# Optimization experiments

Hardware: AMD Instinct MI355X
Metric: run time of the kernel (lower is better)

## Reference

```python
import jax, jax.numpy as jnp
import numpy as np

G = 4          # groups
K = 3          # kernel_size
INC = 64       # channels


def conv3x3(x, w):
    # x: (B, Cin, H, W), w: (Cout, Cin, 3, 3), stride 1, pad 1, no bias
    return jax.lax.conv_general_dilated(
        x, w, window_strides=(1, 1), padding=[(1, 1), (1, 1)],
        dimension_numbers=("NCHW", "OIHW", "NCHW"))


def pconv(x, w):
    # partial conv: 3x3 conv on first C//4 channels, rest untouched
    dc = x.shape[1] // 4
    x1 = conv3x3(x[:, :dc], w)
    return jnp.concatenate([x1, x[:, dc:]], axis=1)


def conv1x1(x, w, b):
    # w: (Cout, Cin), b: (Cout,)
    return jnp.einsum("bchw,oc->bohw", x, w) + b[None, :, None, None]


def deform_sample(img, offset, mask_sig, dilation):
    """Modulated deformable sampling (DSMv3): for each output pixel and each of
    the K*K kernel taps, bilinearly sample img at p + dilated_tap + offset and
    modulate by the (sigmoided) mask. Returns (B, Cg, K*K, H, W)."""
    b, cg, H, W = img.shape
    K2 = K * K
    off = offset.reshape(b, K2, 2, H, W)  # (dy, dx) per tap
    ky = jnp.repeat(jnp.arange(K), K).astype(img.dtype)   # (K2,) row of tap
    kx = jnp.tile(jnp.arange(K), K).astype(img.dtype)     # (K2,) col of tap
    # padding = center*dilation so sampling grid is centered: p = i + (k-1)*dil
    base_y = jnp.arange(H, dtype=img.dtype)[None, :, None] + ((ky - 1.0) * dilation)[:, None, None]  # (K2,H,1)
    base_x = jnp.arange(W, dtype=img.dtype)[None, None, :] + ((kx - 1.0) * dilation)[:, None, None]  # (K2,1,W)
    py = base_y[None] + off[:, :, 0]  # (B,K2,H,W)
    px = base_x[None] + off[:, :, 1]  # (B,K2,H,W)

    y0 = jnp.floor(py)
    x0 = jnp.floor(px)
    wy = py - y0
    wx = px - x0
    imgf = img.reshape(b, cg, H * W)

    def corner(yi, xi, wgt):
        valid = ((yi >= 0) & (yi <= H - 1) & (xi >= 0) & (xi <= W - 1)).astype(img.dtype)
        yc = jnp.clip(yi, 0, H - 1).astype(jnp.int32)
        xc = jnp.clip(xi, 0, W - 1).astype(jnp.int32)
        flat = (yc * W + xc).reshape(b, 1, -1)  # (B,1,K2*H*W)
        v = jnp.take_along_axis(imgf, flat, axis=2).reshape(b, cg, K2, H, W)
        return v * (wgt * valid).reshape(b, 1, K2, H, W)

    val = (corner(y0, x0, (1 - wy) * (1 - wx))
           + corner(y0, x0 + 1, (1 - wy) * wx)
           + corner(y0 + 1, x0, wy * (1 - wx))
           + corner(y0 + 1, x0 + 1, wy * wx))
    return val * mask_sig[:, None]  # (B,Cg,K2,H,W)


def setup_inputs() -> dict:
    key = jax.random.key(0)
    ks = jax.random.split(key, 8)
    dc = INC // 4
    x = jax.random.normal(ks[0], (4, INC, 128, 128), dtype=jnp.float32)
    y = jax.random.normal(ks[1], (8, INC, 128, 128), dtype=jnp.float32)
    # learned params (small random so offsets stay near-zero, as after training warmup)
    offset_pconv_w = jax.random.normal(ks[2], (G, dc, dc, 3, 3), dtype=jnp.float32) * 0.1
    offset_w = jax.random.normal(ks[3], (G, 2 * K * K, INC), dtype=jnp.float32) * 0.1
    offset_b = jax.random.normal(ks[4], (G, 2 * K * K), dtype=jnp.float32) * 0.1
    mask_pconv_w = jax.random.normal(ks[5], (dc, dc, 3, 3), dtype=jnp.float32) * 0.1
    mask_w = jax.random.normal(ks[6], (K * K, INC), dtype=jnp.float32) * 0.1
    mask_b = jax.random.normal(ks[7], (K * K,), dtype=jnp.float32) * 0.1
    return {"x": x, "y": y,
            "offset_pconv_w": offset_pconv_w, "offset_w": offset_w, "offset_b": offset_b,
            "mask_pconv_w": mask_pconv_w, "mask_w": mask_w, "mask_b": mask_b}


def reference(x, y, offset_pconv_w, offset_w, offset_b, mask_pconv_w, mask_w, mask_b):
    b, c, h, w = x.shape
    cg = c // G
    mask = jax.nn.sigmoid(conv1x1(pconv(x, mask_pconv_w), mask_w, mask_b))  # (B,K2,H,W), shared
    y1, y2 = jnp.split(y, 2, axis=0)
    outs1, outs2 = [], []
    for g in range(G):
        offset = conv1x1(pconv(x, offset_pconv_w[g]), offset_w[g], offset_b[g])  # (B,2*K2,H,W)
        dil = 2 * g + 1
        outs1.append(deform_sample(y1[:, g * cg:(g + 1) * cg], offset, mask, dil))
        outs2.append(deform_sample(y2[:, g * cg:(g + 1) * cg], offset, mask, dil))
    y1n = jnp.concatenate(outs1, axis=1)  # (B,C,K2,H,W)
    y2n = jnp.concatenate(outs2, axis=1)
    return jnp.concatenate([y1n, y2n], axis=0)  # (2B,C,K2,H,W)
```

## Files before the change

### kernel.cpp

```cpp
#include <hip/hip_runtime.h>
#include <hip/hip_bf16.h>
#include <math.h>

constexpr int HH   = 128;
constexpr int WW   = 128;
constexpr int HWsz = HH * WW;

constexpr long OFFS_OFF = 0;
constexpr long MASK_OFF = OFFS_OFF + 4L * 4 * 18 * HWsz;
constexpr long WEO_OFF  = MASK_OFF + 4L * 9 * HWsz;
constexpr long WRO_OFF  = WEO_OFF + 4L * 16 * 9 * 18;
constexpr long WEM_OFF  = WRO_OFF + 4L * 48 * 18;
constexpr long WRM_OFF  = WEM_OFF + 16L * 9 * 9;

__global__ __launch_bounds__(256) void prep_kernel(
    const float* __restrict__ off_pw,
    const float* __restrict__ off_w,
    const float* __restrict__ mask_pw,
    const float* __restrict__ mask_w,
    float* __restrict__ Weff_off, float* __restrict__ Wraw_off,
    float* __restrict__ Weff_mask, float* __restrict__ Wraw_mask)
{
    const int i = blockIdx.x * 256 + threadIdx.x;
    if (i < 10368) {
        const int o = i % 18; int r = i / 18;
        const int t = r % 9;  r /= 9;
        const int ci = r % 16; const int g = r / 16;
        float s = 0.f;
        for (int co = 0; co < 16; ++co)
            s += off_w[(g * 18 + o) * 64 + co] *
                 off_pw[((g * 16 + co) * 16 + ci) * 9 + t];
        Weff_off[i] = s;
    } else if (i < 10368 + 3456) {
        const int j = i - 10368;
        const int o = j % 18; int r = j / 18;
        const int c = r % 48; const int g = r / 48;
        Wraw_off[j] = off_w[(g * 18 + o) * 64 + 16 + c];
    } else if (i < 10368 + 3456 + 1296) {
        const int j = i - 13824;
        const int o = j % 9; int r = j / 9;
        const int t = r % 9; const int ci = r / 9;
        float s = 0.f;
        for (int co = 0; co < 16; ++co)
            s += mask_w[o * 64 + co] * mask_pw[((co * 16) + ci) * 9 + t];
        Weff_mask[j] = s;
    } else if (i < 10368 + 3456 + 1296 + 432) {
        const int j = i - 15120;
        const int o = j % 9; const int c = j / 9;
        Wraw_mask[j] = mask_w[o * 64 + 16 + c];
    }
}

__global__ __launch_bounds__(256) void field_kernel(
    const float* __restrict__ x,
    const float* __restrict__ Weff_off, const float* __restrict__ Wraw_off,
    const float* __restrict__ off_b,
    const float* __restrict__ Weff_mask, const float* __restrict__ Wraw_mask,
    const float* __restrict__ mask_b,
    float* __restrict__ offs, float* __restrict__ maskf)
{
    const int p    = blockIdx.x * 256 + threadIdx.x;
    const int bx   = blockIdx.y;
    const int pass = blockIdx.z;
    const int h = p >> 7, w = p & 127;
    const float* xb = x + (long)bx * 64 * HWsz;

    if (pass < 4) {
        const int g = pass;
        float acc[18];
        #pragma unroll
        for (int o = 0; o < 18; ++o) acc[o] = off_b[g * 18 + o];
        for (int ci = 0; ci < 16; ++ci) {
            const float* xp = xb + ci * HWsz;
            #pragma unroll
            for (int t = 0; t < 9; ++t) {
                const int hh = h + t / 3 - 1, w2 = w + t % 3 - 1;
                float xv = 0.f;
                if ((unsigned)hh < 128u && (unsigned)w2 < 128u)
                    xv = xp[hh * 128 + w2];
                const float* wp = Weff_off + ((g * 16 + ci) * 9 + t) * 18;
                #pragma unroll
                for (int o = 0; o < 18; ++o) acc[o] = fmaf(xv, wp[o], acc[o]);
            }
        }
        for (int c = 0; c < 48; ++c) {
            const float xv = xb[(16 + c) * HWsz + p];
            const float* wp = Wraw_off + (g * 48 + c) * 18;
            #pragma unroll
            for (int o = 0; o < 18; ++o) acc[o] = fmaf(xv, wp[o], acc[o]);
        }
        float* op = offs + ((long)(bx * 4 + g) * 18) * HWsz + p;
        #pragma unroll
        for (int o = 0; o < 18; ++o) op[(long)o * HWsz] = acc[o];
    } else {
        float acc[9];
        #pragma unroll
        for (int o = 0; o < 9; ++o) acc[o] = mask_b[o];
        for (int ci = 0; ci < 16; ++ci) {
            const float* xp = xb + ci * HWsz;
            #pragma unroll
            for (int t = 0; t < 9; ++t) {
                const int hh = h + t / 3 - 1, w2 = w + t % 3 - 1;
                float xv = 0.f;
                if ((unsigned)hh < 128u && (unsigned)w2 < 128u)
                    xv = xp[hh * 128 + w2];
                const float* wp = Weff_mask + (ci * 9 + t) * 9;
                #pragma unroll
                for (int o = 0; o < 9; ++o) acc[o] = fmaf(xv, wp[o], acc[o]);
            }
        }
        for (int c = 0; c < 48; ++c) {
            const float xv = xb[(16 + c) * HWsz + p];
            const float* wp = Wraw_mask + c * 9;
            #pragma unroll
            for (int o = 0; o < 9; ++o) acc[o] = fmaf(xv, wp[o], acc[o]);
        }
        float* op = maskf + (long)bx * 9 * HWsz + p;
        #pragma unroll
        for (int o = 0; o < 9; ++o)
            op[(long)o * HWsz] = 1.0f / (1.0f + __expf(-acc[o]));
    }
}

__global__ __launch_bounds__(256) void sample_kernel(
    const float* __restrict__ y,
    const float* __restrict__ offs,
    const float* __restrict__ maskf,
    float* __restrict__ out)
{
    const int p  = blockIdx.x * 256 + threadIdx.x;
    const int bg = blockIdx.y;
    const int bx = bg >> 2, g = bg & 3;
    const int k  = blockIdx.z;
    const int h = p >> 7, w = p & 127;
    const int dil = 2 * g + 1;

    const long obase = ((long)(bx * 4 + g) * 18) * HWsz + p;
    const float dy = offs[obase + (long)(2 * k) * HWsz];
    const float dx = offs[obase + (long)(2 * k + 1) * HWsz];
    const float m  = maskf[((long)bx * 9 + k) * HWsz + p];

    const float py = (float)(h + (k / 3 - 1) * dil) + dy;
    const float px = (float)(w + (k % 3 - 1) * dil) + dx;
    const float y0f = floorf(py), x0f = floorf(px);
    const float wy = py - y0f, wx = px - x0f;
    const int y0 = (int)y0f, x0 = (int)x0f;
    const int y1 = y0 + 1, x1 = x0 + 1;
    const bool vy0 = (unsigned)y0 < 128u, vy1 = (unsigned)y1 < 128u;
    const bool vx0 = (unsigned)x0 < 128u, vx1 = (unsigned)x1 < 128u;
    const float a00 = (vy0 && vx0) ? (1.f - wy) * (1.f - wx) * m : 0.f;
    const float a01 = (vy0 && vx1) ? (1.f - wy) * wx * m : 0.f;
    const float a10 = (vy1 && vx0) ? wy * (1.f - wx) * m : 0.f;
    const float a11 = (vy1 && vx1) ? wy * wx * m : 0.f;
    const int yc0 = min(max(y0, 0), 127), yc1 = min(max(y1, 0), 127);
    const int xc0 = min(max(x0, 0), 127), xc1 = min(max(x1, 0), 127);
    const int i00 = yc0 * 128 + xc0, i01 = yc0 * 128 + xc1;
    const int i10 = yc1 * 128 + xc0, i11 = yc1 * 128 + xc1;

    #pragma unroll
    for (int half = 0; half < 2; ++half) {
        const int b2 = bx + half * 4;
        const float* yp = y + (long)(b2 * 64 + g * 16) * HWsz;
        float* op = out + ((long)(b2 * 64 + g * 16) * 9 + k) * HWsz + p;
        #pragma unroll
        for (int ci = 0; ci < 16; ++ci) {
            const float* pl = yp + (long)ci * HWsz;
            const float v = fmaf(pl[i00], a00,
                             fmaf(pl[i01], a01,
                              fmaf(pl[i10], a10, pl[i11] * a11)));
            op[(long)ci * 9 * HWsz] = v;
        }
    }
}

extern "C" void kernel_launch(void* const* d_in, const int* in_sizes, int n_in,
                              void* d_out, int out_size, void* d_ws, size_t ws_size,
                              hipStream_t stream) {
    const float* x       = (const float*)d_in[0];
    const float* y       = (const float*)d_in[1];
    const float* off_pw  = (const float*)d_in[2];
    const float* off_w   = (const float*)d_in[3];
    const float* off_b   = (const float*)d_in[4];
    const float* mask_pw = (const float*)d_in[5];
    const float* mask_w  = (const float*)d_in[6];
    const float* mask_b  = (const float*)d_in[7];
    float* out = (float*)d_out;

    float* ws        = (float*)d_ws;
    float* offs      = ws + OFFS_OFF;
    float* maskf     = ws + MASK_OFF;
    float* Weff_off  = ws + WEO_OFF;
    float* Wraw_off  = ws + WRO_OFF;
    float* Weff_mask = ws + WEM_OFF;
    float* Wraw_mask = ws + WRM_OFF;

    prep_kernel<<<61, 256, 0, stream>>>(off_pw, off_w, mask_pw, mask_w,
                                        Weff_off, Wraw_off, Weff_mask, Wraw_mask);
    field_kernel<<<dim3(64, 4, 5), 256, 0, stream>>>(
        x, Weff_off, Wraw_off, off_b, Weff_mask, Wraw_mask, mask_b, offs, maskf);
    sample_kernel<<<dim3(64, 16, 9), 256, 0, stream>>>(y, offs, maskf, out);
}
```

Baseline: 538.0 us.

## Transpose field weights, reorder sample grid, use nontemporal loads and stores

Transposes the precomputed 3x3 effective weights to an (o, t) layout so the field kernel loads all nine neighbour values first and then runs contiguous FMAs per output, with the ci loops kept rolled. The sample kernel becomes a flat 1D grid whose block order puts the 16 batch-group combos for one tile and tap next to each other, which should improve cache reuse of y planes and offsets. Offset and mask reads and output writes now use nontemporal hints to keep the large write-once output from evicting the gathered y data from cache. The main cost targeted is memory traffic in the output-bound sample kernel, while the field-kernel change is minor.

```diff
diff --git a/kernel.cpp b/kernel.cpp
--- a/kernel.cpp
+++ b/kernel.cpp
@@ -2,35 +2,33 @@
 #include <hip/hip_bf16.h>
 #include <math.h>
 
-constexpr int HH   = 128;
-constexpr int WW   = 128;
-constexpr int HWsz = HH * WW;
+constexpr int HWsz = 128 * 128;
 
 constexpr long OFFS_OFF = 0;
 constexpr long MASK_OFF = OFFS_OFF + 4L * 4 * 18 * HWsz;
-constexpr long WEO_OFF  = MASK_OFF + 4L * 9 * HWsz;
-constexpr long WRO_OFF  = WEO_OFF + 4L * 16 * 9 * 18;
-constexpr long WEM_OFF  = WRO_OFF + 4L * 48 * 18;
-constexpr long WRM_OFF  = WEM_OFF + 16L * 9 * 9;
+constexpr long WTO_OFF  = MASK_OFF + 4L * 9 * HWsz;
+constexpr long WRO_OFF  = WTO_OFF + 4L * 16 * 18 * 9;
+constexpr long WTM_OFF  = WRO_OFF + 4L * 48 * 18;
+constexpr long WRM_OFF  = WTM_OFF + 16L * 9 * 9;
 
 __global__ __launch_bounds__(256) void prep_kernel(
     const float* __restrict__ off_pw,
     const float* __restrict__ off_w,
     const float* __restrict__ mask_pw,
     const float* __restrict__ mask_w,
-    float* __restrict__ Weff_off, float* __restrict__ Wraw_off,
-    float* __restrict__ Weff_mask, float* __restrict__ Wraw_mask)
+    float* __restrict__ WT_off, float* __restrict__ Wraw_off,
+    float* __restrict__ WT_mask, float* __restrict__ Wraw_mask)
 {
     const int i = blockIdx.x * 256 + threadIdx.x;
     if (i < 10368) {
-        const int o = i % 18; int r = i / 18;
-        const int t = r % 9;  r /= 9;
+        const int t = i % 9; int r = i / 9;
+        const int o = r % 18; r /= 18;
         const int ci = r % 16; const int g = r / 16;
         float s = 0.f;
         for (int co = 0; co < 16; ++co)
             s += off_w[(g * 18 + o) * 64 + co] *
                  off_pw[((g * 16 + co) * 16 + ci) * 9 + t];
-        Weff_off[i] = s;
+        WT_off[i] = s;
     } else if (i < 10368 + 3456) {
         const int j = i - 10368;
         const int o = j % 18; int r = j / 18;
@@ -38,12 +36,12 @@
         Wraw_off[j] = off_w[(g * 18 + o) * 64 + 16 + c];
     } else if (i < 10368 + 3456 + 1296) {
         const int j = i - 13824;
-        const int o = j % 9; int r = j / 9;
-        const int t = r % 9; const int ci = r / 9;
+        const int t = j % 9; int r = j / 9;
+        const int o = r % 9; const int ci = r / 9;
         float s = 0.f;
         for (int co = 0; co < 16; ++co)
-            s += mask_w[o * 64 + co] * mask_pw[((co * 16) + ci) * 9 + t];
-        Weff_mask[j] = s;
+            s += mask_w[o * 64 + co] * mask_pw[(co * 16 + ci) * 9 + t];
+        WT_mask[j] = s;
     } else if (i < 10368 + 3456 + 1296 + 432) {
         const int j = i - 15120;
         const int o = j % 9; const int c = j / 9;
@@ -53,9 +51,9 @@
 
 __global__ __launch_bounds__(256) void field_kernel(
     const float* __restrict__ x,
-    const float* __restrict__ Weff_off, const float* __restrict__ Wraw_off,
+    const float* __restrict__ WT_off, const float* __restrict__ Wraw_off,
     const float* __restrict__ off_b,
-    const float* __restrict__ Weff_mask, const float* __restrict__ Wraw_mask,
+    const float* __restrict__ WT_mask, const float* __restrict__ Wraw_mask,
     const float* __restrict__ mask_b,
     float* __restrict__ offs, float* __restrict__ maskf)
 {
@@ -70,19 +68,25 @@
         float acc[18];
         #pragma unroll
         for (int o = 0; o < 18; ++o) acc[o] = off_b[g * 18 + o];
+        #pragma unroll 1
         for (int ci = 0; ci < 16; ++ci) {
             const float* xp = xb + ci * HWsz;
+            float v[9];
             #pragma unroll
             for (int t = 0; t < 9; ++t) {
                 const int hh = h + t / 3 - 1, w2 = w + t % 3 - 1;
-                float xv = 0.f;
-                if ((unsigned)hh < 128u && (unsigned)w2 < 128u)
-                    xv = xp[hh * 128 + w2];
-                const float* wp = Weff_off + ((g * 16 + ci) * 9 + t) * 18;
+                v[t] = ((unsigned)hh < 128u && (unsigned)w2 < 128u)
+                         ? xp[hh * 128 + w2] : 0.f;
+            }
+            const float* wp = WT_off + (long)(g * 16 + ci) * 18 * 9;
+            #pragma unroll
+            for (int o = 0; o < 18; ++o) {
                 #pragma unroll
-                for (int o = 0; o < 18; ++o) acc[o] = fmaf(xv, wp[o], acc[o]);
-            }
-        }
+                for (int t = 0; t < 9; ++t)
+                    acc[o] = fmaf(v[t], wp[o * 9 + t], acc[o]);
+            }
+        }
+        #pragma unroll 1
         for (int c = 0; c < 48; ++c) {
             const float xv = xb[(16 + c) * HWsz + p];
             const float* wp = Wraw_off + (g * 48 + c) * 18;
@@ -96,19 +100,25 @@
         float acc[9];
         #pragma unroll
         for (int o = 0; o < 9; ++o) acc[o] = mask_b[o];
+        #pragma unroll 1
         for (int ci = 0; ci < 16; ++ci) {
             const float* xp = xb + ci * HWsz;
+            float v[9];
             #pragma unroll
             for (int t = 0; t < 9; ++t) {
                 const int hh = h + t / 3 - 1, w2 = w + t % 3 - 1;
-                float xv = 0.f;
-                if ((unsigned)hh < 128u && (unsigned)w2 < 128u)
-                    xv = xp[hh * 128 + w2];
-                const float* wp = Weff_mask + (ci * 9 + t) * 9;
+                v[t] = ((unsigned)hh < 128u && (unsigned)w2 < 128u)
+                         ? xp[hh * 128 + w2] : 0.f;
+            }
+            const float* wp = WT_mask + (long)ci * 9 * 9;
+            #pragma unroll
+            for (int o = 0; o < 9; ++o) {
                 #pragma unroll
-                for (int o = 0; o < 9; ++o) acc[o] = fmaf(xv, wp[o], acc[o]);
-            }
-        }
+                for (int t = 0; t < 9; ++t)
+                    acc[o] = fmaf(v[t], wp[o * 9 + t], acc[o]);
+            }
+        }
+        #pragma unroll 1
         for (int c = 0; c < 48; ++c) {
             const float xv = xb[(16 + c) * HWsz + p];
             const float* wp = Wraw_mask + c * 9;
@@ -128,17 +138,20 @@
     const float* __restrict__ maskf,
     float* __restrict__ out)
 {
-    const int p  = blockIdx.x * 256 + threadIdx.x;
-    const int bg = blockIdx.y;
+    const int id   = blockIdx.x;
+    const int bg   = id & 15;
+    const int rest = id >> 4;
+    const int tile = rest / 9;
+    const int k    = rest - tile * 9;
+    const int p    = tile * 256 + threadIdx.x;
     const int bx = bg >> 2, g = bg & 3;
-    const int k  = blockIdx.z;
     const int h = p >> 7, w = p & 127;
     const int dil = 2 * g + 1;
 
     const long obase = ((long)(bx * 4 + g) * 18) * HWsz + p;
-    const float dy = offs[obase + (long)(2 * k) * HWsz];
-    const float dx = offs[obase + (long)(2 * k + 1) * HWsz];
-    const float m  = maskf[((long)bx * 9 + k) * HWsz + p];
+    const float dy = __builtin_nontemporal_load(&offs[obase + (long)(2 * k) * HWsz]);
+    const float dx = __builtin_nontemporal_load(&offs[obase + (long)(2 * k + 1) * HWsz]);
+    const float m  = __builtin_nontemporal_load(&maskf[((long)bx * 9 + k) * HWsz + p]);
 
     const float py = (float)(h + (k / 3 - 1) * dil) + dy;
     const float px = (float)(w + (k % 3 - 1) * dil) + dx;
@@ -168,7 +181,7 @@
             const float v = fmaf(pl[i00], a00,
                              fmaf(pl[i01], a01,
                               fmaf(pl[i10], a10, pl[i11] * a11)));
-            op[(long)ci * 9 * HWsz] = v;
+            __builtin_nontemporal_store(v, &op[(long)ci * 9 * HWsz]);
         }
     }
 }
@@ -189,14 +202,14 @@
     float* ws        = (float*)d_ws;
     float* offs      = ws + OFFS_OFF;
     float* maskf     = ws + MASK_OFF;
-    float* Weff_off  = ws + WEO_OFF;
+    float* WT_off    = ws + WTO_OFF;
     float* Wraw_off  = ws + WRO_OFF;
-    float* Weff_mask = ws + WEM_OFF;
+    float* WT_mask   = ws + WTM_OFF;
     float* Wraw_mask = ws + WRM_OFF;
 
     prep_kernel<<<61, 256, 0, stream>>>(off_pw, off_w, mask_pw, mask_w,
-                                        Weff_off, Wraw_off, Weff_mask, Wraw_mask);
+                                        WT_off, Wraw_off, WT_mask, Wraw_mask);
     field_kernel<<<dim3(64, 4, 5), 256, 0, stream>>>(
-        x, Weff_off, Wraw_off, off_b, Weff_mask, Wraw_mask, mask_b, offs, maskf);
-    sample_kernel<<<dim3(64, 16, 9), 256, 0, stream>>>(y, offs, maskf, out);
-}
+        x, WT_off, Wraw_off, off_b, WT_mask, Wraw_mask, mask_b, offs, maskf);
+    sample_kernel<<<dim3(64 * 16 * 9), 256, 0, stream>>>(y, offs, maskf, out);
+}
```

Result: no change. 544.4 us (+1.2%).
